# Performance work log

Measured on AMD Instinct MI355X. Metric: run time of the kernel, lower is better.

## Reference

```python
import jax, jax.numpy as jnp
import numpy as np

B, N, EP = 128, 1024, 8192          # graphs, nodes/graph, edges/graph
E = B * EP
K1, K2 = 820, 656                   # ceil(0.8*1024), ceil(0.8*820)
H = 120                             # GRU hidden
L = 101                             # target sequence length

def _w(k, shape, s=0.05):
    return jax.random.normal(k, shape, jnp.float32) * s

def setup_inputs():
    ks = jax.random.split(jax.random.key(0), 16)
    rng = np.random.default_rng(0)
    off = np.arange(B)[:, None] * N
    src = (rng.integers(0, N, size=(B, EP)) + off).reshape(-1).astype(np.int32)
    dst = (rng.integers(0, N, size=(B, EP)) + off).reshape(-1).astype(np.int32)
    return dict(
        x=jax.random.normal(ks[0], (B * N, 4), jnp.float32),
        target=jax.random.normal(ks[1], (B, 30, L), jnp.float32),
        edge_src=jnp.asarray(src), edge_dst=jnp.asarray(dst),
        W1_rel=_w(ks[2], (4, 128)), W1_root=_w(ks[3], (4, 128)), b1=jnp.zeros((128,)),
        p1=_w(ks[4], (128,), 1.0),
        W2_rel=_w(ks[5], (128, 128)), W2_root=_w(ks[6], (128, 128)), b2=jnp.zeros((128,)),
        p2=_w(ks[7], (128,), 1.0),
        Wc=_w(ks[8], (128, 30, 3)), bc=jnp.zeros((128,)),
        Wih_f=_w(ks[9], (3 * H, 128)), Whh_f=_w(ks[10], (3 * H, H)),
        bih_f=jnp.zeros((3 * H,)), bhh_f=jnp.zeros((3 * H,)),
        Wih_b=_w(ks[11], (3 * H, 128)), Whh_b=_w(ks[12], (3 * H, H)),
        bih_b=jnp.zeros((3 * H,)), bhh_b=jnp.zeros((3 * H,)),
        Wd1=_w(ks[13], (4816, 102)), bd1=jnp.zeros((102,)),
        Wd3=_w(ks[14], (102, 2)), bd3=jnp.zeros((2,)),
    )

def _gconv(x, src, dst, valid, n, Wrel, Wroot, b):
    # PyG GraphConv: lin_rel(sum_{j->i} x_j) + lin_root(x_i)
    m = x[src] * valid[:, None]                       # [E,F] gather + edge mask
    agg = jax.ops.segment_sum(m, dst, num_segments=n)  # scatter-add
    return agg @ Wrel + x @ Wroot + b

def _topk_pool(x, src, dst, valid, n_per, k, p):
    # PyG TopKPooling: score = tanh(x.p/||p||); keep top-k per graph; x *= score
    score = jnp.tanh(x @ p / jnp.linalg.norm(p))      # [B*n_per]
    _, idx = jax.lax.top_k(score.reshape(B, n_per), k)
    perm = (idx + jnp.arange(B)[:, None] * n_per).reshape(-1)  # [B*k] global ids
    new_x = x[perm] * score[perm][:, None]
    mapping = jnp.full((B * n_per,), -1, jnp.int32).at[perm].set(
        jnp.arange(B * k, dtype=jnp.int32))
    ns, nd = mapping[src], mapping[dst]
    nv = valid & (ns >= 0) & (nd >= 0)                # edges with both ends kept
    return new_x, jnp.maximum(ns, 0), jnp.maximum(nd, 0), nv

def _readout(x, k):
    xr = x.reshape(B, k, 128)
    return jnp.concatenate([xr.max(1), xr.mean(1)], axis=1)  # gmp || gap -> [B,256]

def _gru_dir(xs, Wih, Whh, bih, bhh):                 # xs: [T,B,128]
    def step(h, xt):
        gi = xt @ Wih.T + bih
        gh = h @ Whh.T + bhh
        ir, iz, inn = jnp.split(gi, 3, -1)
        hr, hz, hn = jnp.split(gh, 3, -1)
        r = jax.nn.sigmoid(ir + hr)
        z = jax.nn.sigmoid(iz + hz)
        ng = jnp.tanh(inn + r * hn)
        hnew = (1.0 - z) * ng + z * h
        return hnew, hnew
    h0 = jnp.zeros((xs.shape[1], H), xs.dtype)
    return jax.lax.scan(step, h0, xs)[1]              # [T,B,H]

def _forward(params, edge_src, edge_dst):
    (x, target, W1_rel, W1_root, b1, p1, W2_rel, W2_root, b2, p2, Wc, bc,
     Wih_f, Whh_f, bih_f, bhh_f, Wih_b, Whh_b, bih_b, bhh_b,
     Wd1, bd1, Wd3, bd3) = params
    valid0 = jnp.ones((E,), bool)
    h = jax.nn.relu(_gconv(x, edge_src, edge_dst, valid0, B * N, W1_rel, W1_root, b1))
    h, s1, d1, v1 = _topk_pool(h, edge_src, edge_dst, valid0, N, K1, p1)
    x1 = _readout(h, K1)
    h = jax.nn.relu(_gconv(h, s1, d1, v1, B * K1, W2_rel, W2_root, b2))
    h, s2, d2, v2 = _topk_pool(h, s1, d1, v1, K1, K2, p2)
    x2 = _readout(h, K2)
    xg = x1 + x2                                      # [B,256]
    # target branch (dropout = identity in eval mode)
    xt = jax.lax.conv_general_dilated(target, Wc, (1,), 'VALID',
                                      dimension_numbers=('NCH', 'OIH', 'NCH'))
    xt = jax.nn.relu(xt + bc[None, :, None])          # [B,128,99]
    xt = xt[:, :, :95].reshape(B, 128, 19, 5).mean(-1)  # avg_pool1d(k=5,s=5)
    xs = xt.transpose(2, 0, 1)                        # [T=19,B,128]
    yf = _gru_dir(xs, Wih_f, Whh_f, bih_f, bhh_f)
    yb = _gru_dir(xs[::-1], Wih_b, Whh_b, bih_b, bhh_b)[::-1]
    y = jnp.concatenate([yf, yb], -1).transpose(1, 0, 2).reshape(B, -1)  # [B,4560]
    xc = jnp.concatenate([xg, y], 1)                  # [B,4816]
    xc = jax.nn.relu(xc @ Wd1 + bd1)
    return jax.nn.log_softmax(xc @ Wd3 + bd3, axis=-1)

def reference(x, target, edge_src, edge_dst, W1_rel, W1_root, b1, p1,
              W2_rel, W2_root, b2, p2, Wc, bc, Wih_f, Whh_f, bih_f, bhh_f,
              Wih_b, Whh_b, bih_b, bhh_b, Wd1, bd1, Wd3, bd3):
    params = (x, target, W1_rel, W1_root, b1, p1, W2_rel, W2_root, b2, p2,
              Wc, bc, Wih_f, Whh_f, bih_f, bhh_f, Wih_b, Whh_b, bih_b, bhh_b,
              Wd1, bd1, Wd3, bd3)
    return _forward(params, edge_src, edge_dst)
```

## Files before the change

### kernel.cpp

```cpp
#include <hip/hip_runtime.h>
#include <math.h>

#define BB   128
#define NN   1024
#define BN   (BB*NN)
#define EDG  (BB*8192)
#define K1C  820
#define K2C  656
#define TSEQ 19
#define HID  120
#define D1K  4816
#define D1CH 76
#define NCH2 11

typedef unsigned short u16;
typedef __attribute__((ext_vector_type(8))) short bf16x8;
typedef __attribute__((ext_vector_type(4))) float f32x4;

__device__ __forceinline__ u16 f2b(float x) {
  unsigned int u = __float_as_uint(x);
  u += 0x7FFFu + ((u >> 16) & 1u);
  return (u16)(u >> 16);
}
__device__ __forceinline__ float b2f(u16 v) {
  return __uint_as_float(((unsigned int)v) << 16);
}

__device__ __forceinline__ float blockReduceSum128(float v, float* tmp2) {
#pragma unroll
  for (int o = 32; o > 0; o >>= 1) v += __shfl_down(v, o);
  int lane = threadIdx.x & 63, w = threadIdx.x >> 6;
  if (lane == 0) tmp2[w] = v;
  __syncthreads();
  float r = tmp2[0] + tmp2[1];
  __syncthreads();
  return r;
}

__global__ void k_pnorm(const float* __restrict__ p1, const float* __restrict__ p2,
                        float* __restrict__ invp) {
  __shared__ float tmp2[2];
  float a = p1[threadIdx.x], b = p2[threadIdx.x];
  float s1 = blockReduceSum128(a * a, tmp2);
  float s2 = blockReduceSum128(b * b, tmp2);
  if (threadIdx.x == 0) { invp[0] = 1.f / sqrtf(s1); invp[1] = 1.f / sqrtf(s2); }
}

__global__ void k_wb(const float* __restrict__ W2rel, const float* __restrict__ W2root,
                     u16* __restrict__ Wfrag) {
  int idx = blockIdx.x * 256 + threadIdx.x;
  int lane = idx & 63, ct = (idx >> 6) & 7, ks = idx >> 9;
  int c = ct * 16 + (lane & 15);
  int kbase = ks * 32 + (lane >> 4) * 8;
#pragma unroll
  for (int j = 0; j < 8; ++j) {
    int k = kbase + j;
    float w = (k < 128) ? W2rel[(size_t)k * 128 + c] : W2root[(size_t)(k - 128) * 128 + c];
    Wfrag[(size_t)idx * 8 + j] = f2b(w);
  }
}

__global__ __launch_bounds__(1024) void k_l1(const int* __restrict__ src,
                                             const int* __restrict__ dst,
                                             const float* __restrict__ x,
                                             float* __restrict__ agg1) {
  __shared__ int hcur[1024];
  __shared__ int sscan[1024];
  __shared__ int ccnt[1024];
  __shared__ int el[8192];
  __shared__ float4 xls4[1024];
  int b = blockIdx.x, tid = threadIdx.x;
  int base = b * 8192, nb = b * 1024;
  hcur[tid] = 0;
  __syncthreads();
#pragma unroll
  for (int it = 0; it < 8; ++it)
    atomicAdd(&hcur[dst[base + it * 1024 + tid] - nb], 1);
  __syncthreads();
  int v = hcur[tid];
  ccnt[tid] = v;
  sscan[tid] = v;
  __syncthreads();
  for (int o = 1; o < 1024; o <<= 1) {
    int t = (tid >= o) ? sscan[tid - o] : 0;
    __syncthreads();
    sscan[tid] += t;
    __syncthreads();
  }
  hcur[tid] = sscan[tid] - v;
  __syncthreads();
#pragma unroll
  for (int it = 0; it < 8; ++it) {
    int e = base + it * 1024 + tid;
    int d = dst[e] - nb;
    int pos = atomicAdd(&hcur[d], 1);
    el[pos] = src[e] - nb;
  }
  xls4[tid] = ((const float4*)x)[nb + tid];
  __syncthreads();
  const float* xls = (const float*)xls4;
  int rg = tid >> 2, lane = tid & 3;
#pragma unroll
  for (int it = 0; it < 4; ++it) {
    int r = rg + it * 256;
    int n = ccnt[r], s0 = sscan[r] - n;
    float a0 = 0.f, a1 = 0.f;
    int j = 0;
    for (; j + 1 < n; j += 2) {
      a0 += xls[el[s0 + j] * 4 + lane];
      a1 += xls[el[s0 + j + 1] * 4 + lane];
    }
    if (j < n) a0 += xls[el[s0 + j] * 4 + lane];
    agg1[(size_t)(nb + r) * 4 + lane] = a0 + a1;
  }
}

__global__ void k_h1(const float* __restrict__ x, const float* __restrict__ agg1,
                     const float* __restrict__ W1rel, const float* __restrict__ W1root,
                     const float* __restrict__ b1, const float* __restrict__ p1,
                     const float* __restrict__ invp,
                     float* __restrict__ h1, float* __restrict__ score1) {
  int tid = blockIdx.x * 256 + threadIdx.x;
  int r = tid >> 5, lane = tid & 31, f4 = lane * 4;
  float4 a = ((const float4*)agg1)[r];
  float4 xv = ((const float4*)x)[r];
  float o[4], dot = 0.f;
#pragma unroll
  for (int j = 0; j < 4; ++j) {
    int f = f4 + j;
    float acc = b1[f]
      + a.x * W1rel[f] + a.y * W1rel[128 + f] + a.z * W1rel[256 + f] + a.w * W1rel[384 + f]
      + xv.x * W1root[f] + xv.y * W1root[128 + f] + xv.z * W1root[256 + f] + xv.w * W1root[384 + f];
    o[j] = fmaxf(acc, 0.f);
    dot += o[j] * p1[f];
  }
  *(float4*)&h1[(size_t)r * 128 + f4] = make_float4(o[0], o[1], o[2], o[3]);
#pragma unroll
  for (int off = 16; off > 0; off >>= 1) dot += __shfl_down(dot, off, 32);
  if (lane == 0) score1[r] = tanhf(dot * invp[0]);
}

__global__ void k_sort(const float* __restrict__ score, int n_per, int K,
                       int* __restrict__ perm, int* __restrict__ mapping) {
  __shared__ float s[1024];
  __shared__ int   id[1024];
  int b = blockIdx.x;
  const float* sc = score + (size_t)b * n_per;
  for (int i = threadIdx.x; i < 1024; i += blockDim.x) {
    if (i < n_per) { s[i] = sc[i]; id[i] = i; }
    else           { s[i] = -INFINITY; id[i] = 0x7fffffff; }
  }
  __syncthreads();
  for (int k = 2; k <= 1024; k <<= 1) {
    for (int j = k >> 1; j > 0; j >>= 1) {
      for (int i = threadIdx.x; i < 1024; i += blockDim.x) {
        int l = i ^ j;
        if (l > i) {
          float si = s[i], sl = s[l];
          int ii = id[i], il = id[l];
          bool iBeforeL = (si > sl) || (si == sl && ii < il);
          bool up = ((i & k) == 0);
          if (up ? (!iBeforeL) : iBeforeL) {
            s[i] = sl; s[l] = si; id[i] = il; id[l] = ii;
          }
        }
      }
      __syncthreads();
    }
  }
  for (int r = threadIdx.x; r < K; r += blockDim.x)
    perm[(size_t)b * K + r] = b * n_per + id[r];
  if (mapping) {
    for (int i = threadIdx.x; i < n_per; i += blockDim.x)
      mapping[(size_t)b * n_per + i] = -1;
    __syncthreads();
    for (int r = threadIdx.x; r < K; r += blockDim.x)
      mapping[(size_t)b * n_per + id[r]] = b * K + r;
  }
}

#define RCH 64
__global__ void k_gatherread(const u16* __restrict__ h2b, const float* __restrict__ score,
                             const int* __restrict__ perm,
                             float* __restrict__ pmax, float* __restrict__ psum,
                             int K, int nch) {
  int b = blockIdx.x / nch, c = blockIdx.x % nch, f = threadIdx.x;
  int r0 = c * RCH, r1 = min(r0 + RCH, K);
  float mx = -INFINITY, sm = 0.f;
  for (int r = r0; r < r1; ++r) {
    int g = perm[(size_t)b * K + r];
    float v = b2f(h2b[(size_t)g * 128 + f]) * score[g];
    mx = fmaxf(mx, v); sm += v;
  }
  pmax[((size_t)b * nch + c) * 128 + f] = mx;
  psum[((size_t)b * nch + c) * 128 + f] = sm;
}

__global__ __launch_bounds__(1024) void k_csr2(const int* __restrict__ src,
                                               const int* __restrict__ dst,
                                               const int* __restrict__ map,
                                               int* __restrict__ starts2,
                                               int* __restrict__ cnt2,
                                               int* __restrict__ elist2) {
  __shared__ int mloc[8192];
  __shared__ int msl[8192];
  __shared__ int h[1024];
  __shared__ int s[1024];
  int g = blockIdx.x, tid = threadIdx.x;
  int base = g * 8192, nb2 = g * K1C;
  h[tid] = 0;
  __syncthreads();
#pragma unroll
  for (int it = 0; it < 8; ++it) {
    int e = base + it * 1024 + tid;
    int ms = map[src[e]], md = map[dst[e]];
    bool valid = (ms >= 0) && (md >= 0);
    int idx = it * 1024 + tid;
    int ml = valid ? (md - nb2) : -1;
    mloc[idx] = ml;
    msl[idx] = ms - nb2;
    if (valid) atomicAdd(&h[ml], 1);
  }
  __syncthreads();
  int v = (tid < K1C) ? h[tid] : 0;
  if (tid < K1C) cnt2[nb2 + tid] = v;
  s[tid] = v;
  __syncthreads();
  for (int o = 1; o < 1024; o <<= 1) {
    int t = (tid >= o) ? s[tid - o] : 0;
    __syncthreads();
    s[tid] += t;
    __syncthreads();
  }
  int st = s[tid] - v;
  if (tid < K1C) starts2[nb2 + tid] = base + st;
  h[tid] = st;
  __syncthreads();
#pragma unroll
  for (int it = 0; it < 8; ++it) {
    int idx = it * 1024 + tid;
    int ml = mloc[idx];
    if (ml >= 0) {
      int pos = atomicAdd(&h[ml], 1);
      elist2[base + pos] = msl[idx];
    }
  }
}

__global__ __launch_bounds__(1024) void k_agg2r(const int* __restrict__ starts2,
                                                const int* __restrict__ cnt2,
                                                const int* __restrict__ elist2,
                                                const int* __restrict__ perm1,
                                                const float* __restrict__ score1,
                                                const float* __restrict__ h1,
                                                u16* __restrict__ Abf,
                                                float* __restrict__ xmax1,
                                                float* __restrict__ xsum1) {
  __shared__ float xls[K1C * 32];
  __shared__ int   el[8192];
  __shared__ int   sts[K1C];
  __shared__ int   ctn[K1C];
  __shared__ int   pid[K1C];
  __shared__ float scs[K1C];
  __shared__ float red[64][33];
  int g = blockIdx.x >> 2, q = blockIdx.x & 3;
  int tid = threadIdx.x;
  int nb2 = g * K1C, base = g * 8192;
  for (int i = tid; i < K1C; i += 1024) {
    int p = perm1[nb2 + i];
    pid[i] = p;
    scs[i] = score1[p];
    sts[i] = starts2[nb2 + i] - base;
    ctn[i] = cnt2[nb2 + i];
  }
  {
    const int4* e4 = (const int4*)(elist2 + base);
    for (int i = tid; i < 2048; i += 1024) ((int4*)el)[i] = e4[i];
  }
  __syncthreads();
  for (int i = tid; i < K1C * 8; i += 1024) {
    int row = i >> 3, f4 = (i & 7) * 4;
    float4 v = *(const float4*)&h1[(size_t)pid[row] * 128 + q * 32 + f4];
    float s = scs[row];
    v.x *= s; v.y *= s; v.z *= s; v.w *= s;
    *(float4*)&xls[row * 32 + f4] = v;
    ushort4 bv;
    bv.x = f2b(v.x); bv.y = f2b(v.y); bv.z = f2b(v.z); bv.w = f2b(v.w);
    *(ushort4*)&Abf[(size_t)(nb2 + row) * 256 + 128 + q * 32 + f4] = bv;
  }
  __syncthreads();
  int rg = tid >> 4, f2 = (tid & 15) * 2;
  float mx0 = -INFINITY, mx1 = -INFINITY, sm0 = 0.f, sm1 = 0.f;
  for (int r = rg; r < K1C; r += 64) {
    int s0 = sts[r], n = ctn[r];
    float a0 = 0.f, a1 = 0.f, c0 = 0.f, c1 = 0.f;
    int j = 0;
    for (; j + 1 < n; j += 2) {
      float2 v0 = *(const float2*)&xls[el[s0 + j] * 32 + f2];
      float2 v1 = *(const float2*)&xls[el[s0 + j + 1] * 32 + f2];
      a0 += v0.x; a1 += v0.y; c0 += v1.x; c1 += v1.y;
    }
    if (j < n) {
      float2 v = *(const float2*)&xls[el[s0 + j] * 32 + f2];
      a0 += v.x; a1 += v.y;
    }
    ushort2 ov;
    ov.x = f2b(a0 + c0); ov.y = f2b(a1 + c1);
    *(ushort2*)&Abf[(size_t)(nb2 + r) * 256 + q * 32 + f2] = ov;
    float2 w = *(const float2*)&xls[r * 32 + f2];
    mx0 = fmaxf(mx0, w.x); mx1 = fmaxf(mx1, w.y);
    sm0 += w.x; sm1 += w.y;
  }
  red[rg][f2] = mx0; red[rg][f2 + 1] = mx1;
  __syncthreads();
  if (tid < 32) {
    float m = red[0][tid];
#pragma unroll 8
    for (int t2 = 1; t2 < 64; ++t2) m = fmaxf(m, red[t2][tid]);
    xmax1[g * 128 + q * 32 + tid] = m;
  }
  __syncthreads();
  red[rg][f2] = sm0; red[rg][f2 + 1] = sm1;
  __syncthreads();
  if (tid < 32) {
    float s2 = red[0][tid];
#pragma unroll 8
    for (int t2 = 1; t2 < 64; ++t2) s2 += red[t2][tid];
    xsum1[g * 128 + q * 32 + tid] = s2;
  }
}

__global__ __launch_bounds__(256, 4) void k_h2m(
    const u16* __restrict__ Abf, const u16* __restrict__ Wfrag,
    const float* __restrict__ b2, const float* __restrict__ p2,
    const float* __restrict__ invp,
    u16* __restrict__ h2b, float* __restrict__ score2) {
  __shared__ u16 Als[64][40];
  int tid = threadIdx.x;
  int r0 = blockIdx.x * 64;
  int wv = tid >> 6, lane = tid & 63;
  int lr = lane & 15, kg = lane >> 4;
  f32x4 acc[8];
  f32x4 z = {0.f, 0.f, 0.f, 0.f};
#pragma unroll
  for (int ct = 0; ct < 8; ++ct) acc[ct] = z;
  for (int ks = 0; ks < 8; ++ks) {
    {
      int row = tid >> 2, kq = (tid & 3) * 8;
      *(f32x4*)&Als[row][kq] =
          *(const f32x4*)&Abf[(size_t)(r0 + row) * 256 + ks * 32 + kq];
    }
    __syncthreads();
    bf16x8 a = *(const bf16x8*)&Als[wv * 16 + lr][kg * 8];
    const u16* wf = Wfrag + (size_t)ks * 4096;
#pragma unroll
    for (int ct = 0; ct < 8; ++ct) {
      bf16x8 b = *(const bf16x8*)&wf[(ct * 64 + lane) * 8];
      acc[ct] = __builtin_amdgcn_mfma_f32_16x16x32_bf16(a, b, acc[ct], 0, 0, 0);
    }
    __syncthreads();
  }
  float inv = invp[1];
  float dots[4] = {0.f, 0.f, 0.f, 0.f};
#pragma unroll
  for (int ct = 0; ct < 8; ++ct) {
    int c = ct * 16 + lr;
    float bb = b2[c], pp = p2[c];
#pragma unroll
    for (int i = 0; i < 4; ++i) {
      float o = fmaxf(acc[ct][i] + bb, 0.f);
      h2b[(size_t)(r0 + wv * 16 + kg * 4 + i) * 128 + c] = f2b(o);
      dots[i] += o * pp;
    }
  }
#pragma unroll
  for (int i = 0; i < 4; ++i) {
    float d = dots[i];
#pragma unroll
    for (int m = 8; m >= 1; m >>= 1) d += __shfl_xor(d, m);
    if (lr == 0) score2[r0 + wv * 16 + kg * 4 + i] = tanhf(d * inv);
  }
}

__global__ void k_conv(const float* __restrict__ target, const float* __restrict__ Wc,
                       const float* __restrict__ bc, float* __restrict__ xs) {
  int gb = blockIdx.x;
  int b = gb / TSEQ, tt = gb % TSEQ;
  int o = threadIdx.x;
  __shared__ float tg[30][8];
  for (int i = threadIdx.x; i < 210; i += 128) {
    int ch = i / 7, u = i % 7;
    tg[ch][u] = target[((size_t)b * 30 + ch) * 101 + tt * 5 + u];
  }
  __syncthreads();
  const float* w = Wc + (size_t)o * 90;
  float acc5[5] = {0, 0, 0, 0, 0};
  for (int ch = 0; ch < 30; ++ch) {
    float w0 = w[ch * 3], w1 = w[ch * 3 + 1], w2 = w[ch * 3 + 2];
#pragma unroll
    for (int u = 0; u < 5; ++u)
      acc5[u] += tg[ch][u] * w0 + tg[ch][u + 1] * w1 + tg[ch][u + 2] * w2;
  }
  float bo = bc[o], s = 0.f;
#pragma unroll
  for (int u = 0; u < 5; ++u) s += fmaxf(acc5[u] + bo, 0.f);
  xs[((size_t)tt * BB + b) * 128 + o] = s * 0.2f;
}

#define GIB 16
__global__ __launch_bounds__(384) void k_gi(const float* __restrict__ xs,
                     const float* __restrict__ Wihf, const float* __restrict__ bihf,
                     const float* __restrict__ Wihb, const float* __restrict__ bihb,
                     float* __restrict__ gi) {
  int bg = blockIdx.x & 7;
  int t = (blockIdx.x >> 3) % TSEQ;
  int dir = blockIdx.x / (8 * TSEQ);
  int b0 = bg * GIB;
  __shared__ float xst[GIB][128];
  int tid = threadIdx.x;
  for (int i = tid; i < GIB * 128; i += 384) {
    int bb = i >> 7, k = i & 127;
    xst[bb][k] = xs[((size_t)t * BB + b0 + bb) * 128 + k];
  }
  __syncthreads();
  int j = tid;
  if (j < 360) {
    const float* W = (dir ? Wihb : Wihf) + (size_t)j * 128;
    float bias = (dir ? bihb : bihf)[j];
    float acc[GIB];
#pragma unroll
    for (int bb = 0; bb < GIB; ++bb) acc[bb] = bias;
#pragma unroll 4
    for (int k = 0; k < 128; ++k) {
      float w = W[k];
#pragma unroll
      for (int bb = 0; bb < GIB; ++bb) acc[bb] += xst[bb][k] * w;
    }
    size_t base = ((size_t)dir * TSEQ + t) * BB + b0;
#pragma unroll
    for (int bb = 0; bb < GIB; ++bb) gi[(base + bb) * 360 + j] = acc[bb];
  }
}

__global__ __launch_bounds__(384) void k_gru(const float* __restrict__ gi,
                      const float* __restrict__ Whhf, const float* __restrict__ bhhf,
                      const float* __restrict__ Whhb, const float* __restrict__ bhhb,
                      float* __restrict__ xc) {
  int pair = blockIdx.x & 63, dir = blockIdx.x >> 6;
  int b0 = pair * 2;
  const float* Whh = dir ? Whhb : Whhf;
  const float* bhh = dir ? bhhb : bhhf;
  __shared__ float h_sh[2][HID];
  __shared__ float g0[360], g1[360];
  int j = threadIdx.x;
  float wrow[HID];
  float bias = 0.f;
  if (j < 360) {
    const float4* W4 = (const float4*)(Whh + (size_t)j * HID);
#pragma unroll
    for (int k4 = 0; k4 < HID / 4; ++k4) {
      float4 w = W4[k4];
      wrow[k4 * 4 + 0] = w.x; wrow[k4 * 4 + 1] = w.y;
      wrow[k4 * 4 + 2] = w.z; wrow[k4 * 4 + 3] = w.w;
    }
    bias = bhh[j];
  }
  if (j < 2 * HID) h_sh[j / HID][j % HID] = 0.f;
  __syncthreads();
  for (int st = 0; st < TSEQ; ++st) {
    int tt = dir ? (TSEQ - 1 - st) : st;
    if (j < 360) {
      float a0 = bias, a1 = bias;
      const float4* h40 = (const float4*)h_sh[0];
      const float4* h41 = (const float4*)h_sh[1];
#pragma unroll
      for (int k4 = 0; k4 < HID / 4; ++k4) {
        float4 v0 = h40[k4];
        float4 v1 = h41[k4];
        a0 += wrow[k4*4+0]*v0.x + wrow[k4*4+1]*v0.y + wrow[k4*4+2]*v0.z + wrow[k4*4+3]*v0.w;
        a1 += wrow[k4*4+0]*v1.x + wrow[k4*4+1]*v1.y + wrow[k4*4+2]*v1.z + wrow[k4*4+3]*v1.w;
      }
      g0[j] = a0; g1[j] = a1;
    }
    __syncthreads();
    if (j < 2 * HID) {
      int bb = j / HID, th = j - bb * HID;
      const float* g = gi + (((size_t)dir * TSEQ + tt) * BB + (b0 + bb)) * 360;
      const float* gh = bb ? g1 : g0;
      float r  = 1.f / (1.f + expf(-(g[th]       + gh[th])));
      float z  = 1.f / (1.f + expf(-(g[120 + th] + gh[120 + th])));
      float ng = tanhf(g[240 + th] + r * gh[240 + th]);
      float hn = (1.f - z) * ng + z * h_sh[bb][th];
      h_sh[bb][th] = hn;
      xc[(size_t)(b0 + bb) * 4816 + 256 + (size_t)tt * 240 + dir * 120 + th] = hn;
    }
    __syncthreads();
  }
}

__global__ void k_xg(const float* __restrict__ xmax1, const float* __restrict__ xsum1,
                     const float* __restrict__ pmax2, const float* __restrict__ psum2,
                     float* __restrict__ xc) {
  int b = blockIdx.x, f = threadIdx.x;
  float mx2 = -INFINITY, sm2 = 0.f;
  for (int c = 0; c < NCH2; ++c) {
    mx2 = fmaxf(mx2, pmax2[((size_t)b * NCH2 + c) * 128 + f]);
    sm2 += psum2[((size_t)b * NCH2 + c) * 128 + f];
  }
  xc[(size_t)b * 4816 + f] = xmax1[b * 128 + f] + mx2;
  xc[(size_t)b * 4816 + 128 + f] = xsum1[b * 128 + f] / (float)K1C + sm2 / (float)K2C;
}

__global__ __launch_bounds__(128) void k_d1(const float* __restrict__ xc,
                                            const float* __restrict__ Wd1,
                                            float* __restrict__ part) {
  int c = blockIdx.x % D1CH;
  int rg = blockIdx.x / D1CH;
  int k0 = c * 64, kn = min(64, D1K - k0);
  __shared__ float wls[64 * 102];
  __shared__ float xcs[4][64];
  int tid = threadIdx.x;
  for (int i = tid; i < 4 * 64; i += 128) {
    int r = i >> 6, k = i & 63;
    xcs[r][k] = (k < kn) ? xc[(size_t)(rg * 4 + r) * D1K + k0 + k] : 0.f;
  }
  {
    const float2* s2 = (const float2*)(Wd1 + (size_t)k0 * 102);
    float2* d2 = (float2*)wls;
    int n2 = (kn * 102) >> 1;
    for (int i = tid; i < n2; i += 128) d2[i] = s2[i];
  }
  __syncthreads();
  int j = tid;
  if (j < 102) {
    float a0 = 0.f, a1 = 0.f, a2 = 0.f, a3 = 0.f;
#pragma unroll 4
    for (int k = 0; k < kn; ++k) {
      float w = wls[k * 102 + j];
      a0 += xcs[0][k] * w; a1 += xcs[1][k] * w;
      a2 += xcs[2][k] * w; a3 += xcs[3][k] * w;
    }
    part[((size_t)(rg * 4 + 0) * D1CH + c) * 102 + j] = a0;
    part[((size_t)(rg * 4 + 1) * D1CH + c) * 102 + j] = a1;
    part[((size_t)(rg * 4 + 2) * D1CH + c) * 102 + j] = a2;
    part[((size_t)(rg * 4 + 3) * D1CH + c) * 102 + j] = a3;
  }
}

__global__ void k_final2(const float* __restrict__ part, const float* __restrict__ bd1,
                         const float* __restrict__ Wd3, const float* __restrict__ bd3,
                         float* __restrict__ out) {
  __shared__ float tmp2[2];
  int b = blockIdx.x, j = threadIdx.x;
  float v = 0.f;
  if (j < 102) {
    const float* pb = part + (size_t)b * D1CH * 102 + j;
    float s0 = 0.f, s1 = 0.f, s2 = 0.f, s3 = 0.f;
    for (int c = 0; c < D1CH; c += 4) {
      s0 += pb[(c + 0) * 102];
      s1 += pb[(c + 1) * 102];
      s2 += pb[(c + 2) * 102];
      s3 += pb[(c + 3) * 102];
    }
    v = fmaxf((s0 + s1) + (s2 + s3) + bd1[j], 0.f);
  }
  float c0 = (j < 102) ? v * Wd3[j * 2] : 0.f;
  float c1 = (j < 102) ? v * Wd3[j * 2 + 1] : 0.f;
  float z0 = blockReduceSum128(c0, tmp2) + bd3[0];
  float z1 = blockReduceSum128(c1, tmp2) + bd3[1];
  if (j < 2) {
    float m = fmaxf(z0, z1);
    float lse = m + logf(expf(z0 - m) + expf(z1 - m));
    out[b * 2 + j] = (j == 0 ? z0 : z1) - lse;
  }
}

extern "C" void kernel_launch(void* const* d_in, const int* in_sizes, int n_in,
                              void* d_out, int out_size, void* d_ws, size_t ws_size,
                              hipStream_t stream) {
  const float* x      = (const float*)d_in[0];
  const float* target = (const float*)d_in[1];
  const int*   esrc   = (const int*)d_in[2];
  const int*   edst   = (const int*)d_in[3];
  const float* W1rel  = (const float*)d_in[4];
  const float* W1root = (const float*)d_in[5];
  const float* b1     = (const float*)d_in[6];
  const float* p1     = (const float*)d_in[7];
  const float* W2rel  = (const float*)d_in[8];
  const float* W2root = (const float*)d_in[9];
  const float* b2     = (const float*)d_in[10];
  const float* p2     = (const float*)d_in[11];
  const float* Wc     = (const float*)d_in[12];
  const float* bc     = (const float*)d_in[13];
  const float* Wihf   = (const float*)d_in[14];
  const float* Whhf   = (const float*)d_in[15];
  const float* bihf   = (const float*)d_in[16];
  const float* bhhf   = (const float*)d_in[17];
  const float* Wihb   = (const float*)d_in[18];
  const float* Whhb   = (const float*)d_in[19];
  const float* bihb   = (const float*)d_in[20];
  const float* bhhb   = (const float*)d_in[21];
  const float* Wd1    = (const float*)d_in[22];
  const float* bd1    = (const float*)d_in[23];
  const float* Wd3    = (const float*)d_in[24];
  const float* bd3    = (const float*)d_in[25];
  float* out = (float*)d_out;

  char* wsb = (char*)d_ws;
  size_t off = 0;
  auto alloc = [&](size_t bytes) -> void* {
    void* p = wsb + off;
    off = (off + bytes + 255) & ~(size_t)255;
    return p;
  };
  float* h1      = (float*)alloc((size_t)BN * 128 * 4);
  u16*   Abf     = (u16*)  alloc((size_t)BB * K1C * 256 * 2);
  u16*   Wfrag   = (u16*)  alloc((size_t)4096 * 8 * 2);
  float* agg1    = (float*)alloc((size_t)BN * 4 * 4);
  float* score1  = (float*)alloc((size_t)BN * 4);
  int*   perm1   = (int*)  alloc((size_t)BB * K1C * 4);
  int*   map1    = (int*)  alloc((size_t)BN * 4);
  u16*   h2b     = (u16*)  alloc((size_t)BB * K1C * 128 * 2);
  float* score2  = (float*)alloc((size_t)BB * K1C * 4);
  int*   perm2   = (int*)  alloc((size_t)BB * K2C * 4);
  float* invp    = (float*)alloc(256);
  float* xs      = (float*)alloc((size_t)TSEQ * BB * 128 * 4);
  float* gi      = (float*)alloc((size_t)2 * TSEQ * BB * 360 * 4);
  float* xc      = (float*)alloc((size_t)BB * 4816 * 4);
  int*   starts2 = (int*)  alloc((size_t)BB * K1C * 4);
  int*   cnt2    = (int*)  alloc((size_t)BB * K1C * 4);
  int*   elist2  = (int*)  alloc((size_t)EDG * 4);
  float* xmax1   = (float*)alloc((size_t)BB * 128 * 4);
  float* xsum1   = (float*)alloc((size_t)BB * 128 * 4);
  float* pmax2   = (float*)alloc((size_t)BB * NCH2 * 128 * 4);
  float* psum2   = (float*)alloc((size_t)BB * NCH2 * 128 * 4);
  float* part    = (float*)alloc((size_t)BB * D1CH * 102 * 4);

  k_pnorm<<<1, 128, 0, stream>>>(p1, p2, invp);
  k_wb<<<16, 256, 0, stream>>>(W2rel, W2root, Wfrag);

  k_l1<<<BB, 1024, 0, stream>>>(esrc, edst, x, agg1);
  k_h1<<<BN * 32 / 256, 256, 0, stream>>>(x, agg1, W1rel, W1root, b1, p1, invp, h1, score1);
  k_sort<<<BB, 512, 0, stream>>>(score1, NN, K1C, perm1, map1);

  k_csr2<<<BB, 1024, 0, stream>>>(esrc, edst, map1, starts2, cnt2, elist2);
  k_agg2r<<<BB * 4, 1024, 0, stream>>>(starts2, cnt2, elist2, perm1, score1, h1,
                                       Abf, xmax1, xsum1);
  k_h2m<<<(BB * K1C) / 64, 256, 0, stream>>>(Abf, Wfrag, b2, p2, invp, h2b, score2);
  k_sort<<<BB, 512, 0, stream>>>(score2, K1C, K2C, perm2, nullptr);
  k_gatherread<<<BB * NCH2, 128, 0, stream>>>(h2b, score2, perm2, pmax2, psum2, K2C, NCH2);

  k_conv<<<BB * TSEQ, 128, 0, stream>>>(target, Wc, bc, xs);
  k_gi<<<2 * TSEQ * 8, 384, 0, stream>>>(xs, Wihf, bihf, Wihb, bihb, gi);
  k_gru<<<2 * 64, 384, 0, stream>>>(gi, Whhf, bhhf, Whhb, bhhb, xc);

  k_xg<<<BB, 128, 0, stream>>>(xmax1, xsum1, pmax2, psum2, xc);
  k_d1<<<(BB / 4) * D1CH, 128, 0, stream>>>(xc, Wd1, part);
  k_final2<<<BB, 128, 0, stream>>>(part, bd1, Wd3, bd3, out);
}
```

Baseline: 308.0 us.

## Widen sort blocks, vectorize agg2 with shuffle reductions, one GRU block per sample

The sort kernel now launches 1024 threads per graph instead of 512, so each bitonic stage takes one pass instead of two. The layer-2 aggregation uses float4 lanes over 8 threads per row, and its max/sum reductions go through wavefront shuffles plus one 16-entry shared-memory stage instead of two 64-row shared reductions. The GRU runs one block per sample and direction (256 blocks instead of 128), which halves the serial dot-product work per block on this 19-step latency-bound recurrence. The cost is that GRU weights are loaded twice as often and each block holds fewer independent FMAs to hide latency.

```diff
diff --git a/kernel.cpp b/kernel.cpp
--- a/kernel.cpp
+++ b/kernel.cpp
@@ -140,7 +140,7 @@
   if (lane == 0) score1[r] = tanhf(dot * invp[0]);
 }
 
-__global__ void k_sort(const float* __restrict__ score, int n_per, int K,
+__global__ __launch_bounds__(1024) void k_sort(const float* __restrict__ score, int n_per, int K,
                        int* __restrict__ perm, int* __restrict__ mapping) {
   __shared__ float s[1024];
   __shared__ int   id[1024];
@@ -262,7 +262,8 @@
   __shared__ int   ctn[K1C];
   __shared__ int   pid[K1C];
   __shared__ float scs[K1C];
-  __shared__ float red[64][33];
+  __shared__ float redm[16][36];
+  __shared__ float reds[16][36];
   int g = blockIdx.x >> 2, q = blockIdx.x & 3;
   int tid = threadIdx.x;
   int nb2 = g * K1C, base = g * 8192;
@@ -289,43 +290,54 @@
     *(ushort4*)&Abf[(size_t)(nb2 + row) * 256 + 128 + q * 32 + f4] = bv;
   }
   __syncthreads();
-  int rg = tid >> 4, f2 = (tid & 15) * 2;
-  float mx0 = -INFINITY, mx1 = -INFINITY, sm0 = 0.f, sm1 = 0.f;
-  for (int r = rg; r < K1C; r += 64) {
+  int rg = tid >> 3, f4l = (tid & 7) * 4;
+  float4 mx = make_float4(-INFINITY, -INFINITY, -INFINITY, -INFINITY);
+  float4 sm = make_float4(0.f, 0.f, 0.f, 0.f);
+  for (int r = rg; r < K1C; r += 128) {
     int s0 = sts[r], n = ctn[r];
-    float a0 = 0.f, a1 = 0.f, c0 = 0.f, c1 = 0.f;
+    float4 a = make_float4(0.f, 0.f, 0.f, 0.f);
+    float4 c = make_float4(0.f, 0.f, 0.f, 0.f);
     int j = 0;
     for (; j + 1 < n; j += 2) {
-      float2 v0 = *(const float2*)&xls[el[s0 + j] * 32 + f2];
-      float2 v1 = *(const float2*)&xls[el[s0 + j + 1] * 32 + f2];
-      a0 += v0.x; a1 += v0.y; c0 += v1.x; c1 += v1.y;
+      float4 v0 = *(const float4*)&xls[el[s0 + j] * 32 + f4l];
+      float4 v1 = *(const float4*)&xls[el[s0 + j + 1] * 32 + f4l];
+      a.x += v0.x; a.y += v0.y; a.z += v0.z; a.w += v0.w;
+      c.x += v1.x; c.y += v1.y; c.z += v1.z; c.w += v1.w;
     }
     if (j < n) {
-      float2 v = *(const float2*)&xls[el[s0 + j] * 32 + f2];
-      a0 += v.x; a1 += v.y;
-    }
-    ushort2 ov;
-    ov.x = f2b(a0 + c0); ov.y = f2b(a1 + c1);
-    *(ushort2*)&Abf[(size_t)(nb2 + r) * 256 + q * 32 + f2] = ov;
-    float2 w = *(const float2*)&xls[r * 32 + f2];
-    mx0 = fmaxf(mx0, w.x); mx1 = fmaxf(mx1, w.y);
-    sm0 += w.x; sm1 += w.y;
-  }
-  red[rg][f2] = mx0; red[rg][f2 + 1] = mx1;
+      float4 v = *(const float4*)&xls[el[s0 + j] * 32 + f4l];
+      a.x += v.x; a.y += v.y; a.z += v.z; a.w += v.w;
+    }
+    ushort4 ov;
+    ov.x = f2b(a.x + c.x); ov.y = f2b(a.y + c.y);
+    ov.z = f2b(a.z + c.z); ov.w = f2b(a.w + c.w);
+    *(ushort4*)&Abf[(size_t)(nb2 + r) * 256 + q * 32 + f4l] = ov;
+    float4 w = *(const float4*)&xls[r * 32 + f4l];
+    mx.x = fmaxf(mx.x, w.x); mx.y = fmaxf(mx.y, w.y);
+    mx.z = fmaxf(mx.z, w.z); mx.w = fmaxf(mx.w, w.w);
+    sm.x += w.x; sm.y += w.y; sm.z += w.z; sm.w += w.w;
+  }
+#pragma unroll
+  for (int m = 8; m <= 32; m <<= 1) {
+    mx.x = fmaxf(mx.x, __shfl_xor(mx.x, m)); mx.y = fmaxf(mx.y, __shfl_xor(mx.y, m));
+    mx.z = fmaxf(mx.z, __shfl_xor(mx.z, m)); mx.w = fmaxf(mx.w, __shfl_xor(mx.w, m));
+    sm.x += __shfl_xor(sm.x, m); sm.y += __shfl_xor(sm.y, m);
+    sm.z += __shfl_xor(sm.z, m); sm.w += __shfl_xor(sm.w, m);
+  }
+  int wv = tid >> 6;
+  if ((tid & 63) < 8) {
+    *(float4*)&redm[wv][f4l] = mx;
+    *(float4*)&reds[wv][f4l] = sm;
+  }
   __syncthreads();
   if (tid < 32) {
-    float m = red[0][tid];
-#pragma unroll 8
-    for (int t2 = 1; t2 < 64; ++t2) m = fmaxf(m, red[t2][tid]);
+    float m = redm[0][tid], s2 = reds[0][tid];
+#pragma unroll
+    for (int w2 = 1; w2 < 16; ++w2) {
+      m = fmaxf(m, redm[w2][tid]);
+      s2 += reds[w2][tid];
+    }
     xmax1[g * 128 + q * 32 + tid] = m;
-  }
-  __syncthreads();
-  red[rg][f2] = sm0; red[rg][f2 + 1] = sm1;
-  __syncthreads();
-  if (tid < 32) {
-    float s2 = red[0][tid];
-#pragma unroll 8
-    for (int t2 = 1; t2 < 64; ++t2) s2 += red[t2][tid];
     xsum1[g * 128 + q * 32 + tid] = s2;
   }
 }
@@ -446,12 +458,11 @@
                       const float* __restrict__ Whhf, const float* __restrict__ bhhf,
                       const float* __restrict__ Whhb, const float* __restrict__ bhhb,
                       float* __restrict__ xc) {
-  int pair = blockIdx.x & 63, dir = blockIdx.x >> 6;
-  int b0 = pair * 2;
+  int b = blockIdx.x & 127, dir = blockIdx.x >> 7;
   const float* Whh = dir ? Whhb : Whhf;
   const float* bhh = dir ? bhhb : bhhf;
-  __shared__ float h_sh[2][HID];
-  __shared__ float g0[360], g1[360];
+  __shared__ float h_sh[HID];
+  __shared__ float g_sh[360];
   int j = threadIdx.x;
   float wrow[HID];
   float bias = 0.f;
@@ -465,34 +476,29 @@
     }
     bias = bhh[j];
   }
-  if (j < 2 * HID) h_sh[j / HID][j % HID] = 0.f;
+  if (j < HID) h_sh[j] = 0.f;
   __syncthreads();
   for (int st = 0; st < TSEQ; ++st) {
     int tt = dir ? (TSEQ - 1 - st) : st;
     if (j < 360) {
-      float a0 = bias, a1 = bias;
-      const float4* h40 = (const float4*)h_sh[0];
-      const float4* h41 = (const float4*)h_sh[1];
+      float a0 = bias;
+      const float4* h4 = (const float4*)h_sh;
 #pragma unroll
       for (int k4 = 0; k4 < HID / 4; ++k4) {
-        float4 v0 = h40[k4];
-        float4 v1 = h41[k4];
+        float4 v0 = h4[k4];
         a0 += wrow[k4*4+0]*v0.x + wrow[k4*4+1]*v0.y + wrow[k4*4+2]*v0.z + wrow[k4*4+3]*v0.w;
-        a1 += wrow[k4*4+0]*v1.x + wrow[k4*4+1]*v1.y + wrow[k4*4+2]*v1.z + wrow[k4*4+3]*v1.w;
       }
-      g0[j] = a0; g1[j] = a1;
-    }
-    __syncthreads();
-    if (j < 2 * HID) {
-      int bb = j / HID, th = j - bb * HID;
-      const float* g = gi + (((size_t)dir * TSEQ + tt) * BB + (b0 + bb)) * 360;
-      const float* gh = bb ? g1 : g0;
-      float r  = 1.f / (1.f + expf(-(g[th]       + gh[th])));
-      float z  = 1.f / (1.f + expf(-(g[120 + th] + gh[120 + th])));
-      float ng = tanhf(g[240 + th] + r * gh[240 + th]);
-      float hn = (1.f - z) * ng + z * h_sh[bb][th];
-      h_sh[bb][th] = hn;
-      xc[(size_t)(b0 + bb) * 4816 + 256 + (size_t)tt * 240 + dir * 120 + th] = hn;
+      g_sh[j] = a0;
+    }
+    __syncthreads();
+    if (j < HID) {
+      const float* g = gi + (((size_t)dir * TSEQ + tt) * BB + b) * 360;
+      float r  = 1.f / (1.f + expf(-(g[j]       + g_sh[j])));
+      float z  = 1.f / (1.f + expf(-(g[120 + j] + g_sh[120 + j])));
+      float ng = tanhf(g[240 + j] + r * g_sh[240 + j]);
+      float hn = (1.f - z) * ng + z * h_sh[j];
+      h_sh[j] = hn;
+      xc[(size_t)b * 4816 + 256 + (size_t)tt * 240 + dir * 120 + j] = hn;
     }
     __syncthreads();
   }
@@ -641,18 +647,18 @@
 
   k_l1<<<BB, 1024, 0, stream>>>(esrc, edst, x, agg1);
   k_h1<<<BN * 32 / 256, 256, 0, stream>>>(x, agg1, W1rel, W1root, b1, p1, invp, h1, score1);
-  k_sort<<<BB, 512, 0, stream>>>(score1, NN, K1C, perm1, map1);
+  k_sort<<<BB, 1024, 0, stream>>>(score1, NN, K1C, perm1, map1);
 
   k_csr2<<<BB, 1024, 0, stream>>>(esrc, edst, map1, starts2, cnt2, elist2);
   k_agg2r<<<BB * 4, 1024, 0, stream>>>(starts2, cnt2, elist2, perm1, score1, h1,
                                        Abf, xmax1, xsum1);
   k_h2m<<<(BB * K1C) / 64, 256, 0, stream>>>(Abf, Wfrag, b2, p2, invp, h2b, score2);
-  k_sort<<<BB, 512, 0, stream>>>(score2, K1C, K2C, perm2, nullptr);
+  k_sort<<<BB, 1024, 0, stream>>>(score2, K1C, K2C, perm2, nullptr);
   k_gatherread<<<BB * NCH2, 128, 0, stream>>>(h2b, score2, perm2, pmax2, psum2, K2C, NCH2);
 
   k_conv<<<BB * TSEQ, 128, 0, stream>>>(target, Wc, bc, xs);
   k_gi<<<2 * TSEQ * 8, 384, 0, stream>>>(xs, Wihf, bihf, Wihb, bihb, gi);
-  k_gru<<<2 * 64, 384, 0, stream>>>(gi, Whhf, bhhf, Whhb, bhhb, xc);
+  k_gru<<<2 * 128, 384, 0, stream>>>(gi, Whhf, bhhf, Whhb, bhhb, xc);
 
   k_xg<<<BB, 128, 0, stream>>>(xmax1, xsum1, pmax2, psum2, xc);
   k_d1<<<(BB / 4) * D1CH, 128, 0, stream>>>(xc, Wd1, part);
```

Result: faster. 273.8 us (median of 2 runs) (-11.1%).
